# Performance work log

Measured on AMD Instinct MI355X. Metric: run time of the kernel, lower is better.

Reference implementation:

```python
import jax, jax.numpy as jnp
import numpy as np

HEADS = 16
D_MODEL = 1024
GROUP = 4
SEQ = 2048
HEAD_DIM = D_MODEL // HEADS          # 64
KV_HEADS = HEADS // GROUP            # 4


def rope_tables(head_dim, seq_len, base=10000.0):
    # NOTE: faithful to source: exp = -2*arange(0,d,2)/d  (steps of 2 -> base^{-4j/d})
    exp = -2.0 * jnp.arange(0, head_dim, 2, dtype=jnp.float32) / head_dim
    thetas = jnp.power(base, exp)                       # [d/2]
    m = jnp.arange(seq_len, dtype=jnp.float32)          # [S]
    freq = jnp.outer(m, thetas)                         # [S, d/2]
    return jnp.cos(freq), jnp.sin(freq)


def apply_rope(x, cos, sin):
    # x: [B,S,H,D]; complex rotation on consecutive pairs
    B, S, H, D = x.shape
    xr = x.reshape(B, S, H, D // 2, 2)
    x0, x1 = xr[..., 0], xr[..., 1]
    c = cos[None, :S, None, :]
    s = sin[None, :S, None, :]
    out = jnp.stack([x0 * c - x1 * s, x0 * s + x1 * c], axis=-1)
    return out.reshape(B, S, H, D)


def setup_inputs() -> dict:
    key = jax.random.key(0)
    ks = jax.random.split(key, 8)
    B = 1
    q = jax.random.normal(ks[0], (B, SEQ, D_MODEL), dtype=jnp.float32)
    k = jax.random.normal(ks[1], (B, SEQ, D_MODEL), dtype=jnp.float32)
    v = jax.random.normal(ks[2], (B, SEQ, D_MODEL), dtype=jnp.float32)
    mask = jnp.tril(jnp.ones((SEQ, SEQ), dtype=jnp.int32))[None]  # causal [B,S,S]
    sc = 0.02
    Wq = jax.random.normal(ks[3], (D_MODEL, D_MODEL), dtype=jnp.float32) * sc
    Wk = jax.random.normal(ks[4], (D_MODEL, D_MODEL // GROUP), dtype=jnp.float32) * sc
    Wv = jax.random.normal(ks[5], (D_MODEL, D_MODEL // GROUP), dtype=jnp.float32) * sc
    Wo = jax.random.normal(ks[6], (D_MODEL, D_MODEL), dtype=jnp.float32) * sc
    bq = jnp.zeros((D_MODEL,), jnp.float32)
    bk = jnp.zeros((D_MODEL // GROUP,), jnp.float32)
    bv = jnp.zeros((D_MODEL // GROUP,), jnp.float32)
    bo = jnp.zeros((D_MODEL,), jnp.float32)
    return {"q": q, "k": k, "v": v, "mask": mask, "Wq": Wq, "bq": bq,
            "Wk": Wk, "bk": bk, "Wv": Wv, "bv": bv, "Wo": Wo, "bo": bo}


def reference(q, k, v, mask, Wq, bq, Wk, bk, Wv, bv, Wo, bo):
    B, S, _ = q.shape
    cos, sin = rope_tables(HEAD_DIM, S)
    qh = (q @ Wq + bq).reshape(B, S, HEADS, HEAD_DIM)
    kh = (k @ Wk + bk).reshape(B, S, KV_HEADS, HEAD_DIM)
    vh = (v @ Wv + bv).reshape(B, S, KV_HEADS, HEAD_DIM)
    qh = apply_rope(qh, cos, sin)
    kh = apply_rope(kh, cos, sin)
    qh = qh.transpose(0, 2, 1, 3)                       # [B,H,S,D]
    kh = kh.transpose(0, 2, 1, 3)                       # [B,Hkv,S,D]
    vh = vh.transpose(0, 2, 1, 3)
    # torch .repeat tiles: query head j attends kv head j % KV_HEADS
    kh = jnp.tile(kh, (1, GROUP, 1, 1))                 # [B,H,S,D]
    vh = jnp.tile(vh, (1, GROUP, 1, 1))
    scores = jnp.einsum('bhqd,bhkd->bhqk', qh, kh) / jnp.sqrt(
        jnp.asarray(HEAD_DIM, dtype=qh.dtype))
    scores = jnp.where(mask[:, None, :, :] == 0, -jnp.inf, scores)
    attn = jax.nn.softmax(scores, axis=-1)
    out = jnp.einsum('bhqk,bhkd->bhqd', attn, vh)
    out = out.transpose(0, 2, 1, 3).reshape(B, S, D_MODEL)
    return out @ Wo + bo
```

## Files before the change

kernel.cpp:

```cpp
#include <hip/hip_runtime.h>
#include <hip/hip_bf16.h>
#include <math.h>


#define SEQ 2048
#define DM 1024
#define HD 64

using u16 = unsigned short;
typedef __attribute__((ext_vector_type(8))) short bf16x8;
typedef __attribute__((ext_vector_type(4))) float f32x4;

#define QSCALE 0.18033688011112042f

__device__ __forceinline__ u16 f2b(float f) {
    union { float f; unsigned int i; } v; v.f = f;
    unsigned int u = v.i;
    return (u16)((u + 0x7fffu + ((u >> 16) & 1u)) >> 16);
}
__device__ __forceinline__ u16 f2b_fast(float f) {
    union { float f; unsigned int i; } v; v.f = f;
    return (u16)((v.i + 0x8000u) >> 16);
}

__global__ __launch_bounds__(256) void prep_kernel(
    const float* __restrict__ qin, const float* __restrict__ kin, const float* __restrict__ vin,
    const float* __restrict__ Wq, const float* __restrict__ Wk,
    const float* __restrict__ Wv, const float* __restrict__ Wo,
    u16* __restrict__ Xq, u16* __restrict__ Xk, u16* __restrict__ Xv,
    u16* __restrict__ Wt, u16* __restrict__ wot, float2* __restrict__ rope)
{
    const int b = blockIdx.x;
    const int t = threadIdx.x;

    if (b < 640) {
        __shared__ short T[64][72];
        const float* W; u16* dst; int N, t0, rowoff;
        if (b < 256)      { W = Wq; dst = Wt;  N = 1024; t0 = b;       rowoff = 0; }
        else if (b < 320) { W = Wk; dst = Wt;  N = 256;  t0 = b - 256; rowoff = 1024; }
        else if (b < 384) { W = Wv; dst = Wt;  N = 256;  t0 = b - 320; rowoff = 1280; }
        else              { W = Wo; dst = wot; N = 1024; t0 = b - 384; rowoff = 0; }
        const int ntn = N >> 6;
        const int k0 = (t0 / ntn) * 64, n0 = (t0 % ntn) * 64;
        const int r = t >> 4, c4 = (t & 15) * 4;
        #pragma unroll
        for (int rr = 0; rr < 4; ++rr) {
            const int k = r + rr * 16;
            float4 w4 = *reinterpret_cast<const float4*>(W + (size_t)(k0 + k) * N + n0 + c4);
            T[c4 + 0][k] = (short)f2b(w4.x);
            T[c4 + 1][k] = (short)f2b(w4.y);
            T[c4 + 2][k] = (short)f2b(w4.z);
            T[c4 + 3][k] = (short)f2b(w4.w);
        }
        __syncthreads();
        const int n = t >> 2, ck = (t & 3) * 16;
        u16* dp = dst + (size_t)(rowoff + n0 + n) * DM + k0 + ck;
        *reinterpret_cast<bf16x8*>(dp)     = *reinterpret_cast<const bf16x8*>(&T[n][ck]);
        *reinterpret_cast<bf16x8*>(dp + 8) = *reinterpret_cast<const bf16x8*>(&T[n][ck + 8]);
    } else if (b < 1408) {
        const int idx = b - 640;
        const int which = idx >> 8;
        const int ib = idx & 255;
        const float* src = (which == 0) ? qin : (which == 1) ? kin : vin;
        u16* dst = (which == 0) ? Xq : (which == 1) ? Xk : Xv;
        const size_t base = (size_t)ib * 8192 + (size_t)t * 32;
        #pragma unroll
        for (int c = 0; c < 4; ++c) {
            float4 x0 = *reinterpret_cast<const float4*>(src + base + c * 8);
            float4 x1 = *reinterpret_cast<const float4*>(src + base + c * 8 + 4);
            bf16x8 o;
            o[0] = (short)f2b(x0.x); o[1] = (short)f2b(x0.y);
            o[2] = (short)f2b(x0.z); o[3] = (short)f2b(x0.w);
            o[4] = (short)f2b(x1.x); o[5] = (short)f2b(x1.y);
            o[6] = (short)f2b(x1.z); o[7] = (short)f2b(x1.w);
            *reinterpret_cast<bf16x8*>(dst + base + c * 8) = o;
        }
    } else {
        const int m = (b - 1408) * 256 + t;
        float2* rp = rope + (size_t)m * 32;
        for (int pi = 0; pi < 32; ++pi) {
            const float theta = exp2f(-0.8304820237f * (float)pi);
            float sn, cs;
            sincosf((float)m * theta, &sn, &cs);
            rp[pi] = make_float2(cs, sn);
        }
    }
}

__global__ __launch_bounds__(256) void proj_mfma(
    const u16* __restrict__ Xq, const u16* __restrict__ Xk, const u16* __restrict__ Xv,
    const u16* __restrict__ Wt,
    const float* __restrict__ bq, const float* __restrict__ bk, const float* __restrict__ bv,
    const float2* __restrict__ rope,
    u16* __restrict__ Qr, u16* __restrict__ Kr, u16* __restrict__ Vrt)
{
    const int n0 = blockIdx.x * 64, m0 = blockIdx.y * 64;
    const int zone = (n0 < 1024) ? 0 : (n0 < 1280) ? 1 : 2;
    const u16* __restrict__ Az = (zone == 0) ? Xq : (zone == 1) ? Xk : Xv;

    __shared__ short As[2][64][72];
    __shared__ short Bs[2][64][72];

    const int t = threadIdx.x;
    const int w = t >> 6, lane = t & 63, lm = lane & 15, quad = lane >> 4;
    const int sr = t >> 2, sc = (t & 3) * 16;

    f32x4 acc[4] = { {0,0,0,0}, {0,0,0,0}, {0,0,0,0}, {0,0,0,0} };

    const u16* ap_ = Az + (size_t)(m0 + sr) * DM + sc;
    const u16* bp_ = Wt + (size_t)(n0 + sr) * DM + sc;
    bf16x8 aR0 = *reinterpret_cast<const bf16x8*>(ap_);
    bf16x8 aR1 = *reinterpret_cast<const bf16x8*>(ap_ + 8);
    bf16x8 bR0 = *reinterpret_cast<const bf16x8*>(bp_);
    bf16x8 bR1 = *reinterpret_cast<const bf16x8*>(bp_ + 8);

    for (int k0 = 0; k0 < DM; k0 += 64) {
        const int buf = (k0 >> 6) & 1;
        *reinterpret_cast<bf16x8*>(&As[buf][sr][sc])     = aR0;
        *reinterpret_cast<bf16x8*>(&As[buf][sr][sc + 8]) = aR1;
        *reinterpret_cast<bf16x8*>(&Bs[buf][sr][sc])     = bR0;
        *reinterpret_cast<bf16x8*>(&Bs[buf][sr][sc + 8]) = bR1;
        if (k0 + 64 < DM) {
            aR0 = *reinterpret_cast<const bf16x8*>(ap_ + k0 + 64);
            aR1 = *reinterpret_cast<const bf16x8*>(ap_ + k0 + 72);
            bR0 = *reinterpret_cast<const bf16x8*>(bp_ + k0 + 64);
            bR1 = *reinterpret_cast<const bf16x8*>(bp_ + k0 + 72);
        }
        __syncthreads();
        bf16x8 af0 = *reinterpret_cast<const bf16x8*>(&As[buf][16 * w + lm][quad * 8]);
        bf16x8 af1 = *reinterpret_cast<const bf16x8*>(&As[buf][16 * w + lm][32 + quad * 8]);
        #pragma unroll
        for (int nb = 0; nb < 4; ++nb) {
            bf16x8 b0 = *reinterpret_cast<const bf16x8*>(&Bs[buf][16 * nb + lm][quad * 8]);
            bf16x8 b1 = *reinterpret_cast<const bf16x8*>(&Bs[buf][16 * nb + lm][32 + quad * 8]);
            acc[nb] = __builtin_amdgcn_mfma_f32_16x16x32_bf16(af0, b0, acc[nb], 0, 0, 0);
            acc[nb] = __builtin_amdgcn_mfma_f32_16x16x32_bf16(af1, b1, acc[nb], 0, 0, 0);
        }
        __syncthreads();
    }

    const float* __restrict__ bias = (zone == 0) ? bq : (zone == 1) ? bk : bv;
    const int nbase = (zone == 0) ? n0 : (zone == 1) ? (n0 - 1024) : (n0 - 1280);
    const int head = nbase >> 6;
    #pragma unroll
    for (int nb = 0; nb < 4; ++nb) {
        const int d = 16 * nb + lm;
        const float bvv = bias[nbase + d];
        float vals[4];
        #pragma unroll
        for (int r = 0; r < 4; ++r) vals[r] = acc[nb][r] + bvv;
        if (zone != 2) {
            const int pi = d >> 1;
            const bool odd = (lm & 1);
            const float sca = (zone == 0) ? QSCALE : 1.0f;
            u16* op = (zone == 0 ? Qr : Kr) + (size_t)head * SEQ * HD;
            #pragma unroll
            for (int r = 0; r < 4; ++r) {
                const int m = m0 + 16 * w + quad * 4 + r;
                const float2 cs2 = rope[(size_t)m * 32 + pi];
                float x  = vals[r];
                float xp = __shfl_xor(x, 1);
                float o  = (odd ? (xp * cs2.y + x * cs2.x)
                                : (x * cs2.x - xp * cs2.y)) * sca;
                op[(size_t)m * HD + d] = f2b(o);
            }
        } else {
            u16* vp = Vrt + ((size_t)head * HD + d) * SEQ;
            #pragma unroll
            for (int r = 0; r < 4; ++r) {
                const int m = m0 + 16 * w + quad * 4 + r;
                const int within = m & 63;
                const int pos = (m & ~63) + 4 * (within & 15) + (within >> 4);
                vp[pos] = f2b(vals[r]);
            }
        }
    }
}

__global__ __launch_bounds__(256) void attn_mfma(
    const u16* __restrict__ Qr, const u16* __restrict__ Kr, const u16* __restrict__ Vrt,
    u16* __restrict__ AO)
{
    const int bid = blockIdx.x;
    const int h  = bid & 15;
    const int qt = (bid < 256) ? (bid >> 4) : 31 - ((bid - 256) >> 4);
    const int kvh = h & 3;

    __shared__ u16 Ks[2][64][72];
    __shared__ u16 Vt[2][64][72];
    __shared__ u16 Ps[4][16][76];

    const int t = threadIdx.x;
    const int w = t >> 6, lane = t & 63, lm = lane & 15, quad = lane >> 4;

    {
        const int row = lane >> 2, c = (lane & 3) * 16;
        const u16* qp = Qr + ((size_t)h * SEQ + qt * 64 + w * 16 + row) * HD + c;
        *reinterpret_cast<bf16x8*>(&Ps[w][row][c])     = *reinterpret_cast<const bf16x8*>(qp);
        *reinterpret_cast<bf16x8*>(&Ps[w][row][c + 8]) = *reinterpret_cast<const bf16x8*>(qp + 8);
    }
    const bf16x8 aq0 = *reinterpret_cast<const bf16x8*>(&Ps[w][lm][quad * 8]);
    const bf16x8 aq1 = *reinterpret_cast<const bf16x8*>(&Ps[w][lm][32 + quad * 8]);

    f32x4 O[4] = { {0,0,0,0}, {0,0,0,0}, {0,0,0,0}, {0,0,0,0} };
    float lp[4] = { 0.f, 0.f, 0.f, 0.f };

    const int srow = t >> 2, sc2 = (t & 3) * 16;
    const u16* kb_ = Kr  + ((size_t)kvh * SEQ + srow) * HD + sc2;
    const u16* vb_ = Vrt + ((size_t)kvh * HD + srow) * SEQ + sc2;
    bf16x8 kR0 = *reinterpret_cast<const bf16x8*>(kb_);
    bf16x8 kR1 = *reinterpret_cast<const bf16x8*>(kb_ + 8);
    bf16x8 vR0 = *reinterpret_cast<const bf16x8*>(vb_);
    bf16x8 vR1 = *reinterpret_cast<const bf16x8*>(vb_ + 8);

    for (int kt = 0; kt <= qt; ++kt) {
        const int buf = kt & 1;
        *reinterpret_cast<bf16x8*>(&Ks[buf][srow][sc2])     = kR0;
        *reinterpret_cast<bf16x8*>(&Ks[buf][srow][sc2 + 8]) = kR1;
        *reinterpret_cast<bf16x8*>(&Vt[buf][srow][sc2])     = vR0;
        *reinterpret_cast<bf16x8*>(&Vt[buf][srow][sc2 + 8]) = vR1;
        if (kt < qt) {
            kR0 = *reinterpret_cast<const bf16x8*>(kb_ + (size_t)(kt + 1) * 64 * HD);
            kR1 = *reinterpret_cast<const bf16x8*>(kb_ + (size_t)(kt + 1) * 64 * HD + 8);
            vR0 = *reinterpret_cast<const bf16x8*>(vb_ + (size_t)(kt + 1) * 64);
            vR1 = *reinterpret_cast<const bf16x8*>(vb_ + (size_t)(kt + 1) * 64 + 8);
        }
        __syncthreads();

        f32x4 s[4];
        #pragma unroll
        for (int nb = 0; nb < 4; ++nb) {
            bf16x8 b0 = *reinterpret_cast<const bf16x8*>(&Ks[buf][16 * nb + lm][quad * 8]);
            bf16x8 b1 = *reinterpret_cast<const bf16x8*>(&Ks[buf][16 * nb + lm][32 + quad * 8]);
            f32x4 zz = { 0.f, 0.f, 0.f, 0.f };
            zz = __builtin_amdgcn_mfma_f32_16x16x32_bf16(aq0, b0, zz, 0, 0, 0);
            s[nb] = __builtin_amdgcn_mfma_f32_16x16x32_bf16(aq1, b1, zz, 0, 0, 0);
        }

        if (kt == qt) {
            #pragma unroll
            for (int nb = 0; nb < 4; ++nb)
                #pragma unroll
                for (int r = 0; r < 4; ++r)
                    if (16 * nb + lm > 16 * w + quad * 4 + r) s[nb][r] = -INFINITY;
        }

        #pragma unroll
        for (int r = 0; r < 4; ++r) {
            u16 pk[4];
            #pragma unroll
            for (int nb = 0; nb < 4; ++nb) {
                float e = __builtin_amdgcn_exp2f(fminf(s[nb][r], 126.f));
                lp[r] += e;
                pk[nb] = f2b_fast(e);
            }
            *reinterpret_cast<uint2*>(&Ps[w][quad * 4 + r][4 * lm]) =
                *reinterpret_cast<uint2*>(pk);
        }

        const bf16x8 ap0 = *reinterpret_cast<const bf16x8*>(&Ps[w][lm][quad * 8]);
        const bf16x8 ap1 = *reinterpret_cast<const bf16x8*>(&Ps[w][lm][32 + quad * 8]);
        #pragma unroll
        for (int db = 0; db < 4; ++db) {
            bf16x8 v0 = *reinterpret_cast<const bf16x8*>(&Vt[buf][16 * db + lm][quad * 8]);
            bf16x8 v1 = *reinterpret_cast<const bf16x8*>(&Vt[buf][16 * db + lm][32 + quad * 8]);
            O[db] = __builtin_amdgcn_mfma_f32_16x16x32_bf16(ap0, v0, O[db], 0, 0, 0);
            O[db] = __builtin_amdgcn_mfma_f32_16x16x32_bf16(ap1, v1, O[db], 0, 0, 0);
        }
    }

    #pragma unroll
    for (int r = 0; r < 4; ++r) {
        #pragma unroll
        for (int off = 1; off < 16; off <<= 1)
            lp[r] += __shfl_xor(lp[r], off);
        const float inv = 1.0f / lp[r];
        const size_t row = (size_t)(qt * 64 + 16 * w + quad * 4 + r) * DM + (size_t)h * HD;
        #pragma unroll
        for (int db = 0; db < 4; ++db)
            AO[row + 16 * db + lm] = f2b(O[db][r] * inv);
    }
}

__global__ __launch_bounds__(256) void oproj_mfma(
    const u16* __restrict__ AO, const u16* __restrict__ wot,
    const float* __restrict__ bo, float* __restrict__ out)
{
    __shared__ short As[2][64][72];
    __shared__ short Bs[2][64][72];
    const int t = threadIdx.x;
    const int w = t >> 6, lane = t & 63, lm = lane & 15, quad = lane >> 4;
    const int m0 = blockIdx.y * 64, n0 = blockIdx.x * 64;
    const int sr = t >> 2, sc = (t & 3) * 16;

    f32x4 acc[4] = { {0,0,0,0}, {0,0,0,0}, {0,0,0,0}, {0,0,0,0} };

    const u16* ap_ = AO  + (size_t)(m0 + sr) * DM + sc;
    const u16* bp_ = wot + (size_t)(n0 + sr) * DM + sc;
    bf16x8 aR0 = *reinterpret_cast<const bf16x8*>(ap_);
    bf16x8 aR1 = *reinterpret_cast<const bf16x8*>(ap_ + 8);
    bf16x8 bR0 = *reinterpret_cast<const bf16x8*>(bp_);
    bf16x8 bR1 = *reinterpret_cast<const bf16x8*>(bp_ + 8);

    for (int k0 = 0; k0 < DM; k0 += 64) {
        const int buf = (k0 >> 6) & 1;
        *reinterpret_cast<bf16x8*>(&As[buf][sr][sc])     = aR0;
        *reinterpret_cast<bf16x8*>(&As[buf][sr][sc + 8]) = aR1;
        *reinterpret_cast<bf16x8*>(&Bs[buf][sr][sc])     = bR0;
        *reinterpret_cast<bf16x8*>(&Bs[buf][sr][sc + 8]) = bR1;
        if (k0 + 64 < DM) {
            aR0 = *reinterpret_cast<const bf16x8*>(ap_ + k0 + 64);
            aR1 = *reinterpret_cast<const bf16x8*>(ap_ + k0 + 72);
            bR0 = *reinterpret_cast<const bf16x8*>(bp_ + k0 + 64);
            bR1 = *reinterpret_cast<const bf16x8*>(bp_ + k0 + 72);
        }
        __syncthreads();
        bf16x8 af0 = *reinterpret_cast<const bf16x8*>(&As[buf][16 * w + lm][quad * 8]);
        bf16x8 af1 = *reinterpret_cast<const bf16x8*>(&As[buf][16 * w + lm][32 + quad * 8]);
        #pragma unroll
        for (int nb = 0; nb < 4; ++nb) {
            bf16x8 b0 = *reinterpret_cast<const bf16x8*>(&Bs[buf][16 * nb + lm][quad * 8]);
            bf16x8 b1 = *reinterpret_cast<const bf16x8*>(&Bs[buf][16 * nb + lm][32 + quad * 8]);
            acc[nb] = __builtin_amdgcn_mfma_f32_16x16x32_bf16(af0, b0, acc[nb], 0, 0, 0);
            acc[nb] = __builtin_amdgcn_mfma_f32_16x16x32_bf16(af1, b1, acc[nb], 0, 0, 0);
        }
        __syncthreads();
    }

    #pragma unroll
    for (int nb = 0; nb < 4; ++nb) {
        const int dl = 16 * nb + lm;
        const float bv = bo[n0 + dl];
        #pragma unroll
        for (int r = 0; r < 4; ++r) {
            const int m = m0 + 16 * w + quad * 4 + r;
            out[(size_t)m * DM + n0 + dl] = acc[nb][r] + bv;
        }
    }
}

extern "C" void kernel_launch(void* const* d_in, const int* in_sizes, int n_in,
                              void* d_out, int out_size, void* d_ws, size_t ws_size,
                              hipStream_t stream)
{
    const float* q  = (const float*)d_in[0];
    const float* k  = (const float*)d_in[1];
    const float* v  = (const float*)d_in[2];
    const float* Wq = (const float*)d_in[4];
    const float* bq = (const float*)d_in[5];
    const float* Wk = (const float*)d_in[6];
    const float* bk = (const float*)d_in[7];
    const float* Wv = (const float*)d_in[8];
    const float* bv = (const float*)d_in[9];
    const float* Wo = (const float*)d_in[10];
    const float* bo = (const float*)d_in[11];
    float* out = (float*)d_out;

    u16* Xq  = (u16*)d_ws;
    u16* Xk  = Xq  + (size_t)SEQ * DM;
    u16* Xv  = Xk  + (size_t)SEQ * DM;
    u16* Wt  = Xv  + (size_t)SEQ * DM;
    u16* wot = Wt  + (size_t)1536 * 1024;
    u16* Qr  = wot + (size_t)1024 * 1024;
    u16* Kr  = Qr  + (size_t)16 * SEQ * HD;
    u16* Vrt = Kr  + (size_t)4 * SEQ * HD;
    u16* AO  = Vrt + (size_t)4 * SEQ * HD;
    float2* rope = (float2*)(AO + (size_t)SEQ * DM);

    hipLaunchKernelGGL(prep_kernel, dim3(1416), dim3(256), 0, stream,
                       q, k, v, Wq, Wk, Wv, Wo, Xq, Xk, Xv, Wt, wot, rope);
    hipLaunchKernelGGL(proj_mfma, dim3(24, 32), dim3(256), 0, stream,
                       Xq, Xk, Xv, Wt, bq, bk, bv, rope, Qr, Kr, Vrt);
    hipLaunchKernelGGL(attn_mfma, dim3(512), dim3(256), 0, stream,
                       Qr, Kr, Vrt, AO);
    hipLaunchKernelGGL(oproj_mfma, dim3(16, 32), dim3(256), 0, stream,
                       AO, wot, bo, out);
}
```

Baseline: 166.0 us.

## Pre-tile and swizzle projection operands; stage via direct global-to-LDS loads

The prep kernel now writes the bf16 activations and the QKV weight matrices in 64x64 tile-contiguous blocks with an XOR swizzle on 16-byte groups. The projection GEMM can then copy each tile straight into shared memory with global_load_lds instead of going through registers. The XOR-swizzled reads are meant to avoid LDS bank conflicts without padding, and the direct loads cut register traffic and instruction count in the main loop. In exchange the layouts produced by prep and read by the GEMM are tightly coupled, and correctness depends on the async load and barrier ordering, which is not fully visible here.

```diff
diff --git a/kernel.cpp b/kernel.cpp
--- a/kernel.cpp
+++ b/kernel.cpp
@@ -54,26 +54,43 @@
         }
         __syncthreads();
         const int n = t >> 2, ck = (t & 3) * 16;
-        u16* dp = dst + (size_t)(rowoff + n0 + n) * DM + k0 + ck;
-        *reinterpret_cast<bf16x8*>(dp)     = *reinterpret_cast<const bf16x8*>(&T[n][ck]);
-        *reinterpret_cast<bf16x8*>(dp + 8) = *reinterpret_cast<const bf16x8*>(&T[n][ck + 8]);
+        if (b < 384) {
+            const int nt = (rowoff + n0) >> 6, kt = k0 >> 6;
+            char* dp = (char*)(dst + (size_t)(nt * 16 + kt) * 4096) + n * 128;
+            const int g0 = (t & 3) * 2, rx = n & 7;
+            *reinterpret_cast<bf16x8*>(dp + (((g0    ) ^ rx) << 4)) =
+                *reinterpret_cast<const bf16x8*>(&T[n][ck]);
+            *reinterpret_cast<bf16x8*>(dp + (((g0 + 1) ^ rx) << 4)) =
+                *reinterpret_cast<const bf16x8*>(&T[n][ck + 8]);
+        } else {
+            u16* dp = dst + (size_t)(n0 + n) * DM + k0 + ck;
+            *reinterpret_cast<bf16x8*>(dp)     = *reinterpret_cast<const bf16x8*>(&T[n][ck]);
+            *reinterpret_cast<bf16x8*>(dp + 8) = *reinterpret_cast<const bf16x8*>(&T[n][ck + 8]);
+        }
     } else if (b < 1408) {
         const int idx = b - 640;
         const int which = idx >> 8;
         const int ib = idx & 255;
         const float* src = (which == 0) ? qin : (which == 1) ? kin : vin;
         u16* dst = (which == 0) ? Xq : (which == 1) ? Xk : Xv;
-        const size_t base = (size_t)ib * 8192 + (size_t)t * 32;
+        const int m  = ib * 8 + (t >> 5);
+        const int mt = m >> 6, r = m & 63, rx = r & 7;
+        const int col0 = (t & 31) * 32;
+        const float* sp = src + (size_t)m * 1024 + col0;
         #pragma unroll
         for (int c = 0; c < 4; ++c) {
-            float4 x0 = *reinterpret_cast<const float4*>(src + base + c * 8);
-            float4 x1 = *reinterpret_cast<const float4*>(src + base + c * 8 + 4);
+            float4 x0 = *reinterpret_cast<const float4*>(sp + c * 8);
+            float4 x1 = *reinterpret_cast<const float4*>(sp + c * 8 + 4);
             bf16x8 o;
             o[0] = (short)f2b(x0.x); o[1] = (short)f2b(x0.y);
             o[2] = (short)f2b(x0.z); o[3] = (short)f2b(x0.w);
             o[4] = (short)f2b(x1.x); o[5] = (short)f2b(x1.y);
             o[6] = (short)f2b(x1.z); o[7] = (short)f2b(x1.w);
-            *reinterpret_cast<bf16x8*>(dst + base + c * 8) = o;
+            const int col = col0 + c * 8;
+            const int kt = col >> 6, g = (col & 63) >> 3;
+            char* dp = (char*)(dst + (size_t)(mt * 16 + kt) * 4096)
+                     + r * 128 + ((g ^ rx) << 4);
+            *reinterpret_cast<bf16x8*>(dp) = o;
         }
     } else {
         const int m = (b - 1408) * 256 + t;
@@ -98,41 +115,50 @@
     const int zone = (n0 < 1024) ? 0 : (n0 < 1280) ? 1 : 2;
     const u16* __restrict__ Az = (zone == 0) ? Xq : (zone == 1) ? Xk : Xv;
 
-    __shared__ short As[2][64][72];
-    __shared__ short Bs[2][64][72];
+    __shared__ __align__(16) u16 As[2][4096];
+    __shared__ __align__(16) u16 Bs[2][4096];
 
     const int t = threadIdx.x;
     const int w = t >> 6, lane = t & 63, lm = lane & 15, quad = lane >> 4;
-    const int sr = t >> 2, sc = (t & 3) * 16;
 
     f32x4 acc[4] = { {0,0,0,0}, {0,0,0,0}, {0,0,0,0}, {0,0,0,0} };
 
-    const u16* ap_ = Az + (size_t)(m0 + sr) * DM + sc;
-    const u16* bp_ = Wt + (size_t)(n0 + sr) * DM + sc;
-    bf16x8 aR0 = *reinterpret_cast<const bf16x8*>(ap_);
-    bf16x8 aR1 = *reinterpret_cast<const bf16x8*>(ap_ + 8);
-    bf16x8 bR0 = *reinterpret_cast<const bf16x8*>(bp_);
-    bf16x8 bR1 = *reinterpret_cast<const bf16x8*>(bp_ + 8);
-
-    for (int k0 = 0; k0 < DM; k0 += 64) {
-        const int buf = (k0 >> 6) & 1;
-        *reinterpret_cast<bf16x8*>(&As[buf][sr][sc])     = aR0;
-        *reinterpret_cast<bf16x8*>(&As[buf][sr][sc + 8]) = aR1;
-        *reinterpret_cast<bf16x8*>(&Bs[buf][sr][sc])     = bR0;
-        *reinterpret_cast<bf16x8*>(&Bs[buf][sr][sc + 8]) = bR1;
-        if (k0 + 64 < DM) {
-            aR0 = *reinterpret_cast<const bf16x8*>(ap_ + k0 + 64);
-            aR1 = *reinterpret_cast<const bf16x8*>(ap_ + k0 + 72);
-            bR0 = *reinterpret_cast<const bf16x8*>(bp_ + k0 + 64);
-            bR1 = *reinterpret_cast<const bf16x8*>(bp_ + k0 + 72);
-        }
-        __syncthreads();
-        bf16x8 af0 = *reinterpret_cast<const bf16x8*>(&As[buf][16 * w + lm][quad * 8]);
-        bf16x8 af1 = *reinterpret_cast<const bf16x8*>(&As[buf][16 * w + lm][32 + quad * 8]);
+    const char* Ag = (const char*)(Az + (size_t)(m0 >> 6) * 16 * 4096);
+    const char* Bg = (const char*)(Wt + (size_t)(n0 >> 6) * 16 * 4096);
+
+    auto stage = [&](int bufi, int kti) {
+        const char* gA = Ag + (size_t)kti * 8192 + w * 2048 + lane * 16;
+        const char* gB = Bg + (size_t)kti * 8192 + w * 2048 + lane * 16;
+        char* lA = (char*)&As[bufi][0] + w * 2048;
+        char* lB = (char*)&Bs[bufi][0] + w * 2048;
+        #pragma unroll
+        for (int i = 0; i < 2; ++i) {
+            __builtin_amdgcn_global_load_lds(
+                (const __attribute__((address_space(1))) unsigned int*)(gA + i * 1024),
+                (__attribute__((address_space(3))) unsigned int*)(lA + i * 1024), 16, 0, 0);
+            __builtin_amdgcn_global_load_lds(
+                (const __attribute__((address_space(1))) unsigned int*)(gB + i * 1024),
+                (__attribute__((address_space(3))) unsigned int*)(lB + i * 1024), 16, 0, 0);
+        }
+    };
+
+    stage(0, 0);
+    __syncthreads();
+
+    const int rA = 16 * w + lm;
+    const int axr = rA & 7;
+    for (int kt = 0; kt < 16; ++kt) {
+        const int buf = kt & 1;
+        if (kt < 15) stage(buf ^ 1, kt + 1);
+        const char* Ab = (const char*)&As[buf][0];
+        const char* Bb = (const char*)&Bs[buf][0];
+        bf16x8 af0 = *reinterpret_cast<const bf16x8*>(Ab + rA * 128 + (((quad    ) ^ axr) << 4));
+        bf16x8 af1 = *reinterpret_cast<const bf16x8*>(Ab + rA * 128 + (((4 | quad) ^ axr) << 4));
         #pragma unroll
         for (int nb = 0; nb < 4; ++nb) {
-            bf16x8 b0 = *reinterpret_cast<const bf16x8*>(&Bs[buf][16 * nb + lm][quad * 8]);
-            bf16x8 b1 = *reinterpret_cast<const bf16x8*>(&Bs[buf][16 * nb + lm][32 + quad * 8]);
+            const int rB = 16 * nb + lm, bxr = rB & 7;
+            bf16x8 b0 = *reinterpret_cast<const bf16x8*>(Bb + rB * 128 + (((quad    ) ^ bxr) << 4));
+            bf16x8 b1 = *reinterpret_cast<const bf16x8*>(Bb + rB * 128 + (((4 | quad) ^ bxr) << 4));
             acc[nb] = __builtin_amdgcn_mfma_f32_16x16x32_bf16(af0, b0, acc[nb], 0, 0, 0);
             acc[nb] = __builtin_amdgcn_mfma_f32_16x16x32_bf16(af1, b1, acc[nb], 0, 0, 0);
         }
```

After: 165.4 us. About the same (-0.4%).
